# Performance work log

Measured on AMD Instinct MI355X. Metric: run time of the kernel, lower is better.

## Reference

```python
import jax, jax.numpy as jnp
import numpy as np

B, N, H = 4096, 64, 256

def setup_inputs() -> dict:
    key = jax.random.key(0)
    ks = jax.random.split(key, 6)
    scale = 1.0 / np.sqrt(H)
    return {
        "s_t": jax.random.normal(ks[0], (B, H), dtype=jnp.float32),
        "h": jax.random.normal(ks[1], (1, N, H), dtype=jnp.float32) * scale,
        "w": jax.random.normal(ks[2], (1, N, H), dtype=jnp.float32) * scale,
        "U_w": jax.random.normal(ks[3], (H, H), dtype=jnp.float32) * scale,
        "V_w": jax.random.normal(ks[4], (H, H), dtype=jnp.float32) * scale,
        "W_w": jax.random.normal(ks[5], (H, H), dtype=jnp.float32) * scale,
        "prelu_a": jnp.full((1,), 0.25, dtype=jnp.float32),
    }

def _prelu(x, a):
    return jnp.where(x >= 0, x, a * x)

def reference(s_t, h, w, U_w, V_w, W_w, prelu_a):
    # gate: (h + w) @ s_t^T  -> [B, N]
    g = jax.nn.sigmoid(jnp.einsum('onh,bh->bn', h + w, s_t))[..., None]  # [B,N,1]
    # candidate: U(h) + V(w) + W(s_t), broadcast [1,N,H] + [B,1,H] -> [B,N,H]
    cand = _prelu(
        jnp.einsum('onh,kh->onk', h, U_w)
        + jnp.einsum('onh,kh->onk', w, V_w)
        + (s_t @ W_w.T)[:, None, :],
        prelu_a,
    )
    h_new = h + g * cand  # [B,N,H]
    h_new = h_new / jnp.linalg.norm(h_new, axis=2, keepdims=True)
    return h_new
```

## Files before the change

### kernel.cpp

```cpp
#include <hip/hip_runtime.h>
#include <hip/hip_bf16.h>

#define BATCH 4096
#define NMEM  64
#define HDIM  256
#define MROWS 320

typedef __attribute__((ext_vector_type(8))) short short8;
typedef __attribute__((ext_vector_type(4))) float floatx4;

__device__ __forceinline__ float bf2f(unsigned short u) {
    union { unsigned int i; float f; } v; v.i = ((unsigned int)u) << 16; return v.f;
}
__device__ __forceinline__ unsigned short f2bf(float f) {
    union { float f; unsigned int i; } v; v.f = f;
    unsigned int x = v.i;
    return (unsigned short)((x + 0x7FFFu + ((x >> 16) & 1u)) >> 16);
}

__global__ __launch_bounds__(256) void prep_kernel(
    const float* __restrict__ h,
    const float* __restrict__ w,
    const float* __restrict__ U_w,
    const float* __restrict__ V_w,
    const float* __restrict__ W_w,
    unsigned short* __restrict__ M,
    unsigned short* __restrict__ A)
{
    const int bid = blockIdx.x;
    const int t   = threadIdx.x;
    if (bid < 64) {
        const int n = bid;
        __shared__ float h_lds[HDIM];
        __shared__ float w_lds[HDIM];
        h_lds[t] = h[n * HDIM + t];
        w_lds[t] = w[n * HDIM + t];
        __syncthreads();

        const float* Urow = U_w + t * HDIM;
        const float* Vrow = V_w + t * HDIM;
        float acc = 0.f;
        #pragma unroll 8
        for (int hh = 0; hh < HDIM; hh += 4) {
            float4 u = *(const float4*)(Urow + hh);
            float4 v = *(const float4*)(Vrow + hh);
            acc += h_lds[hh + 0] * u.x + h_lds[hh + 1] * u.y
                 + h_lds[hh + 2] * u.z + h_lds[hh + 3] * u.w;
            acc += w_lds[hh + 0] * v.x + w_lds[hh + 1] * v.y
                 + w_lds[hh + 2] * v.z + w_lds[hh + 3] * v.w;
        }
        A[n * HDIM + t] = f2bf(acc);
        M[(256 + n) * HDIM + t] = f2bf(h_lds[t] + w_lds[t]);
    } else {
        const int r0 = (bid - 64) * 4;
        #pragma unroll
        for (int r = 0; r < 4; ++r)
            M[(r0 + r) * HDIM + t] = f2bf(W_w[(r0 + r) * HDIM + t]);
    }
}

__global__ __launch_bounds__(256) void gemm_kernel(
    const float* __restrict__ s_t,
    const unsigned short* __restrict__ M,
    float* __restrict__ Call)
{
    const int b0   = blockIdx.x * 16;
    const int wave = threadIdx.x >> 6;
    const int lane = threadIdx.x & 63;
    const int m = lane & 15;
    const int q = lane >> 4;

    const float* arow = s_t + (size_t)(b0 + m) * HDIM;
    short8 afrag[8];
    #pragma unroll
    for (int ks = 0; ks < 8; ++ks) {
        const int base = ks * 32 + q * 8;
        float4 f0 = *(const float4*)(arow + base);
        float4 f1 = *(const float4*)(arow + base + 4);
        short8 a;
        a[0] = (short)f2bf(f0.x); a[1] = (short)f2bf(f0.y);
        a[2] = (short)f2bf(f0.z); a[3] = (short)f2bf(f0.w);
        a[4] = (short)f2bf(f1.x); a[5] = (short)f2bf(f1.y);
        a[6] = (short)f2bf(f1.z); a[7] = (short)f2bf(f1.w);
        afrag[ks] = a;
    }

    #pragma unroll
    for (int jt = 0; jt < 5; ++jt) {
        const int j0 = (wave + jt * 4) * 16;
        const short8* brow = (const short8*)(M + (size_t)(j0 + m) * HDIM);
        floatx4 acc = {0.f, 0.f, 0.f, 0.f};
        #pragma unroll
        for (int ks = 0; ks < 8; ++ks) {
            short8 bfrag = brow[ks * 4 + q];
            acc = __builtin_amdgcn_mfma_f32_16x16x32_bf16(afrag[ks], bfrag, acc, 0, 0, 0);
        }
        #pragma unroll
        for (int r = 0; r < 4; ++r)
            Call[(size_t)(b0 + q * 4 + r) * MROWS + j0 + m] = acc[r];
    }
}

__global__ __launch_bounds__(256) void fuse_kernel(
    const float* __restrict__ h,
    const unsigned short* __restrict__ A,
    const float* __restrict__ Call,
    const float* __restrict__ prelu_a,
    float* __restrict__ out)
{
    __shared__ unsigned short A_lds[NMEM * HDIM];
    __shared__ float C_lds[8 * HDIM];
    __shared__ float g_lds[8 * NMEM];

    const int t  = threadIdx.x;
    const int b0 = blockIdx.x * 8;
    const float pa = prelu_a[0];

    {
        const ushort4* As = (const ushort4*)A;
        ushort4* Ad = (ushort4*)A_lds;
        #pragma unroll
        for (int i = 0; i < 16; ++i)
            Ad[t + i * 256] = As[t + i * 256];
    }
    #pragma unroll
    for (int b = 0; b < 8; ++b)
        C_lds[b * HDIM + t] = Call[(size_t)(b0 + b) * MROWS + t];
    #pragma unroll
    for (int i = 0; i < 2; ++i) {
        int idx = t + i * 256;
        int b = idx >> 6, n = idx & 63;
        float x = Call[(size_t)(b0 + b) * MROWS + 256 + n];
        g_lds[idx] = 1.f / (1.f + __expf(-x));
    }
    __syncthreads();

    const int wave = t >> 6;
    const int lane = t & 63;
    const int k0 = lane * 4;

    for (int idx = wave; idx < 512; idx += 4) {
        const int b = idx >> 6, n = idx & 63;
        const float g = g_lds[idx];

        ushort4 av = *(const ushort4*)(A_lds + n * HDIM + k0);
        float4  hv = *(const float4*)(h + n * HDIM + k0);
        floatx4 cv = *(const floatx4*)(C_lds + b * HDIM + k0);

        float x0 = bf2f(av.x) + cv[0];
        float x1 = bf2f(av.y) + cv[1];
        float x2 = bf2f(av.z) + cv[2];
        float x3 = bf2f(av.w) + cv[3];
        x0 = (x0 >= 0.f) ? x0 : pa * x0;
        x1 = (x1 >= 0.f) ? x1 : pa * x1;
        x2 = (x2 >= 0.f) ? x2 : pa * x2;
        x3 = (x3 >= 0.f) ? x3 : pa * x3;
        float y0 = hv.x + g * x0;
        float y1 = hv.y + g * x1;
        float y2 = hv.z + g * x2;
        float y3 = hv.w + g * x3;

        float ss = y0 * y0 + y1 * y1 + y2 * y2 + y3 * y3;
        #pragma unroll
        for (int off = 1; off < 64; off <<= 1)
            ss += __shfl_xor(ss, off);
        const float rn = rsqrtf(ss);

        float4 ov;
        ov.x = y0 * rn;
        ov.y = y1 * rn;
        ov.z = y2 * rn;
        ov.w = y3 * rn;
        *(float4*)(out + ((size_t)(b0 + b) * NMEM + n) * HDIM + k0) = ov;
    }
}

extern "C" void kernel_launch(void* const* d_in, const int* in_sizes, int n_in,
                              void* d_out, int out_size, void* d_ws, size_t ws_size,
                              hipStream_t stream) {
    const float* s_t     = (const float*)d_in[0];
    const float* h       = (const float*)d_in[1];
    const float* w       = (const float*)d_in[2];
    const float* U_w     = (const float*)d_in[3];
    const float* V_w     = (const float*)d_in[4];
    const float* W_w     = (const float*)d_in[5];
    const float* prelu_a = (const float*)d_in[6];
    float* out = (float*)d_out;

    unsigned short* M = (unsigned short*)d_ws;
    unsigned short* A = (unsigned short*)((char*)d_ws + MROWS * HDIM * 2);
    float* Call = (float*)((char*)d_ws + MROWS * HDIM * 2 + NMEM * HDIM * 2);

    prep_kernel<<<128, 256, 0, stream>>>(h, w, U_w, V_w, W_w, M, A);
    gemm_kernel<<<BATCH / 16, 256, 0, stream>>>(s_t, M, Call);
    fuse_kernel<<<BATCH / 8, 256, 0, stream>>>(h, A, Call, prelu_a, out);
}
```

Baseline: 316.5 us.

## Use one block per batch in fuse kernel and MFMA for prep matvec

The fuse kernel now runs one block per batch element and reads A and h directly from global memory, no longer staging the whole A matrix in LDS for every block. Each memory row is handled by a 16-lane group, so the sum-of-squares reduction needs four shuffles instead of six. This removes the large per-block LDS fill and raises occupancy, but adds more global or L2 traffic for A and h. The prep kernel computes the U/V projections with bf16 MFMA over fewer blocks, which changes the precision of the input to A, and the h+w rows are folded into the copy blocks.

```diff
diff --git a/kernel.cpp b/kernel.cpp
--- a/kernel.cpp
+++ b/kernel.cpp
@@ -16,6 +16,14 @@
     union { float f; unsigned int i; } v; v.f = f;
     unsigned int x = v.i;
     return (unsigned short)((x + 0x7FFFu + ((x >> 16) & 1u)) >> 16);
+}
+__device__ __forceinline__ short8 pack_bf16x8(float4 f0, float4 f1) {
+    short8 a;
+    a[0] = (short)f2bf(f0.x); a[1] = (short)f2bf(f0.y);
+    a[2] = (short)f2bf(f0.z); a[3] = (short)f2bf(f0.w);
+    a[4] = (short)f2bf(f1.x); a[5] = (short)f2bf(f1.y);
+    a[6] = (short)f2bf(f1.z); a[7] = (short)f2bf(f1.w);
+    return a;
 }
 
 __global__ __launch_bounds__(256) void prep_kernel(
@@ -29,33 +37,43 @@
 {
     const int bid = blockIdx.x;
     const int t   = threadIdx.x;
-    if (bid < 64) {
-        const int n = bid;
-        __shared__ float h_lds[HDIM];
-        __shared__ float w_lds[HDIM];
-        h_lds[t] = h[n * HDIM + t];
-        w_lds[t] = w[n * HDIM + t];
-        __syncthreads();
-
-        const float* Urow = U_w + t * HDIM;
-        const float* Vrow = V_w + t * HDIM;
-        float acc = 0.f;
-        #pragma unroll 8
-        for (int hh = 0; hh < HDIM; hh += 4) {
-            float4 u = *(const float4*)(Urow + hh);
-            float4 v = *(const float4*)(Vrow + hh);
-            acc += h_lds[hh + 0] * u.x + h_lds[hh + 1] * u.y
-                 + h_lds[hh + 2] * u.z + h_lds[hh + 3] * u.w;
-            acc += w_lds[hh + 0] * v.x + w_lds[hh + 1] * v.y
-                 + w_lds[hh + 2] * v.z + w_lds[hh + 3] * v.w;
-        }
-        A[n * HDIM + t] = f2bf(acc);
-        M[(256 + n) * HDIM + t] = f2bf(h_lds[t] + w_lds[t]);
+    if (bid < 16) {
+        const int wv   = t >> 6;
+        const int lane = t & 63;
+        const int m = lane & 15;
+        const int q = lane >> 4;
+        const int j0 = bid * 16;
+
+        const float* ah = h   + (size_t)(wv * 16 + m) * HDIM;
+        const float* aw = w   + (size_t)(wv * 16 + m) * HDIM;
+        const float* bu = U_w + (size_t)(j0 + m) * HDIM;
+        const float* bv = V_w + (size_t)(j0 + m) * HDIM;
+
+        floatx4 acc = {0.f, 0.f, 0.f, 0.f};
+        #pragma unroll
+        for (int ks = 0; ks < 16; ++ks) {
+            const float* asrc = (ks < 8) ? ah : aw;
+            const float* bsrc = (ks < 8) ? bu : bv;
+            const int off = (ks & 7) * 32 + q * 8;
+            float4 a0 = *(const float4*)(asrc + off);
+            float4 a1 = *(const float4*)(asrc + off + 4);
+            float4 b0 = *(const float4*)(bsrc + off);
+            float4 b1 = *(const float4*)(bsrc + off + 4);
+            acc = __builtin_amdgcn_mfma_f32_16x16x32_bf16(
+                pack_bf16x8(a0, a1), pack_bf16x8(b0, b1), acc, 0, 0, 0);
+        }
+        #pragma unroll
+        for (int r = 0; r < 4; ++r)
+            A[(size_t)(wv * 16 + q * 4 + r) * HDIM + j0 + m] = f2bf(acc[r]);
     } else {
-        const int r0 = (bid - 64) * 4;
-        #pragma unroll
-        for (int r = 0; r < 4; ++r)
-            M[(r0 + r) * HDIM + t] = f2bf(W_w[(r0 + r) * HDIM + t]);
+        const int r0 = (bid - 16) * 20;
+        for (int rr = 0; rr < 20; ++rr) {
+            const int r = r0 + rr;
+            float v;
+            if (r < 256) v = W_w[(size_t)r * HDIM + t];
+            else         v = h[(size_t)(r - 256) * HDIM + t] + w[(size_t)(r - 256) * HDIM + t];
+            M[(size_t)r * HDIM + t] = f2bf(v);
+        }
     }
 }
 
@@ -75,14 +93,8 @@
     #pragma unroll
     for (int ks = 0; ks < 8; ++ks) {
         const int base = ks * 32 + q * 8;
-        float4 f0 = *(const float4*)(arow + base);
-        float4 f1 = *(const float4*)(arow + base + 4);
-        short8 a;
-        a[0] = (short)f2bf(f0.x); a[1] = (short)f2bf(f0.y);
-        a[2] = (short)f2bf(f0.z); a[3] = (short)f2bf(f0.w);
-        a[4] = (short)f2bf(f1.x); a[5] = (short)f2bf(f1.y);
-        a[6] = (short)f2bf(f1.z); a[7] = (short)f2bf(f1.w);
-        afrag[ks] = a;
+        afrag[ks] = pack_bf16x8(*(const float4*)(arow + base),
+                                *(const float4*)(arow + base + 4));
     }
 
     #pragma unroll
@@ -108,70 +120,73 @@
     const float* __restrict__ prelu_a,
     float* __restrict__ out)
 {
-    __shared__ unsigned short A_lds[NMEM * HDIM];
-    __shared__ float C_lds[8 * HDIM];
-    __shared__ float g_lds[8 * NMEM];
-
-    const int t  = threadIdx.x;
-    const int b0 = blockIdx.x * 8;
+    __shared__ float C_lds[HDIM];
+    __shared__ float g_lds[NMEM];
+
+    const int t = threadIdx.x;
+    const int b = blockIdx.x;
     const float pa = prelu_a[0];
 
-    {
-        const ushort4* As = (const ushort4*)A;
-        ushort4* Ad = (ushort4*)A_lds;
-        #pragma unroll
-        for (int i = 0; i < 16; ++i)
-            Ad[t + i * 256] = As[t + i * 256];
-    }
-    #pragma unroll
-    for (int b = 0; b < 8; ++b)
-        C_lds[b * HDIM + t] = Call[(size_t)(b0 + b) * MROWS + t];
-    #pragma unroll
-    for (int i = 0; i < 2; ++i) {
-        int idx = t + i * 256;
-        int b = idx >> 6, n = idx & 63;
-        float x = Call[(size_t)(b0 + b) * MROWS + 256 + n];
-        g_lds[idx] = 1.f / (1.f + __expf(-x));
+    C_lds[t] = Call[(size_t)b * MROWS + t];
+    if (t < NMEM) {
+        float x = Call[(size_t)b * MROWS + 256 + t];
+        g_lds[t] = 1.f / (1.f + __expf(-x));
     }
     __syncthreads();
 
     const int wave = t >> 6;
     const int lane = t & 63;
-    const int k0 = lane * 4;
-
-    for (int idx = wave; idx < 512; idx += 4) {
-        const int b = idx >> 6, n = idx & 63;
-        const float g = g_lds[idx];
-
-        ushort4 av = *(const ushort4*)(A_lds + n * HDIM + k0);
-        float4  hv = *(const float4*)(h + n * HDIM + k0);
-        floatx4 cv = *(const floatx4*)(C_lds + b * HDIM + k0);
-
-        float x0 = bf2f(av.x) + cv[0];
-        float x1 = bf2f(av.y) + cv[1];
-        float x2 = bf2f(av.z) + cv[2];
-        float x3 = bf2f(av.w) + cv[3];
-        x0 = (x0 >= 0.f) ? x0 : pa * x0;
-        x1 = (x1 >= 0.f) ? x1 : pa * x1;
-        x2 = (x2 >= 0.f) ? x2 : pa * x2;
-        x3 = (x3 >= 0.f) ? x3 : pa * x3;
-        float y0 = hv.x + g * x0;
-        float y1 = hv.y + g * x1;
-        float y2 = hv.z + g * x2;
-        float y3 = hv.w + g * x3;
-
-        float ss = y0 * y0 + y1 * y1 + y2 * y2 + y3 * y3;
-        #pragma unroll
-        for (int off = 1; off < 64; off <<= 1)
-            ss += __shfl_xor(ss, off);
+    const int qw   = lane >> 4;
+    const int lq   = lane & 15;
+
+    #pragma unroll
+    for (int i = 0; i < 4; ++i) {
+        const int n = i * 16 + wave * 4 + qw;
+        const float g = g_lds[n];
+        const float* hrow = h + (size_t)n * HDIM;
+        const unsigned short* Arow = A + (size_t)n * HDIM;
+
+        float y[16];
+        float ss = 0.f;
+        #pragma unroll
+        for (int j = 0; j < 4; ++j) {
+            const int k = lq * 4 + j * 64;
+            float4  hv = *(const float4*)(hrow + k);
+            ushort4 av = *(const ushort4*)(Arow + k);
+            float4  cv = *(const float4*)(&C_lds[k]);
+            float x0 = bf2f(av.x) + cv.x;
+            float x1 = bf2f(av.y) + cv.y;
+            float x2 = bf2f(av.z) + cv.z;
+            float x3 = bf2f(av.w) + cv.w;
+            x0 = (x0 >= 0.f) ? x0 : pa * x0;
+            x1 = (x1 >= 0.f) ? x1 : pa * x1;
+            x2 = (x2 >= 0.f) ? x2 : pa * x2;
+            x3 = (x3 >= 0.f) ? x3 : pa * x3;
+            float y0 = hv.x + g * x0;
+            float y1 = hv.y + g * x1;
+            float y2 = hv.z + g * x2;
+            float y3 = hv.w + g * x3;
+            y[j * 4 + 0] = y0; y[j * 4 + 1] = y1;
+            y[j * 4 + 2] = y2; y[j * 4 + 3] = y3;
+            ss += y0 * y0 + y1 * y1 + y2 * y2 + y3 * y3;
+        }
+        ss += __shfl_xor(ss, 1);
+        ss += __shfl_xor(ss, 2);
+        ss += __shfl_xor(ss, 4);
+        ss += __shfl_xor(ss, 8);
         const float rn = rsqrtf(ss);
 
-        float4 ov;
-        ov.x = y0 * rn;
-        ov.y = y1 * rn;
-        ov.z = y2 * rn;
-        ov.w = y3 * rn;
-        *(float4*)(out + ((size_t)(b0 + b) * NMEM + n) * HDIM + k0) = ov;
+        float* orow = out + ((size_t)b * NMEM + n) * HDIM;
+        #pragma unroll
+        for (int j = 0; j < 4; ++j) {
+            const int k = lq * 4 + j * 64;
+            float4 ov;
+            ov.x = y[j * 4 + 0] * rn;
+            ov.y = y[j * 4 + 1] * rn;
+            ov.z = y[j * 4 + 2] * rn;
+            ov.w = y[j * 4 + 3] * rn;
+            *(float4*)(orow + k) = ov;
+        }
     }
 }
 
@@ -191,7 +206,7 @@
     unsigned short* A = (unsigned short*)((char*)d_ws + MROWS * HDIM * 2);
     float* Call = (float*)((char*)d_ws + MROWS * HDIM * 2 + NMEM * HDIM * 2);
 
-    prep_kernel<<<128, 256, 0, stream>>>(h, w, U_w, V_w, W_w, M, A);
+    prep_kernel<<<32, 256, 0, stream>>>(h, w, U_w, V_w, W_w, M, A);
     gemm_kernel<<<BATCH / 16, 256, 0, stream>>>(s_t, M, Call);
-    fuse_kernel<<<BATCH / 8, 256, 0, stream>>>(h, A, Call, prelu_a, out);
-}
+    fuse_kernel<<<BATCH, 256, 0, stream>>>(h, A, Call, prelu_a, out);
+}
```

Measured after the change: 305.8 us. -3.4%, faster.
